# Kernel optimization log

Hardware: AMD Instinct MI355X
Metric: run time of the kernel (lower is better)

The kernel has to match this reference:

```python
import jax, jax.numpy as jnp
import numpy as np

G, V_PER, E_PER = 512, 400, 800
N, E = G * V_PER, G * E_PER
NF, H, F, OUT = 128, 64, 8, 64  # n_features, filtration_hidden, n_filtrations, out_dim


def _p(k, shape, fan_in):
    return jax.random.normal(k, shape, jnp.float32) * (1.0 / np.sqrt(fan_in))


def setup_inputs() -> dict:
    key = jax.random.key(0)
    ks = jax.random.split(key, 24)
    x = jax.random.normal(ks[0], (N, NF), jnp.float32)
    pos = jax.random.normal(ks[1], (N, 3), jnp.float32)
    # per-graph random edges, no self loops (dedup'ed single-direction edge list)
    src_l = jax.random.randint(ks[2], (E,), 0, V_PER)
    off = jax.random.randint(ks[3], (E,), 1, V_PER)
    dst_l = (src_l + off) % V_PER
    g = jnp.arange(E, dtype=jnp.int32) // E_PER
    edge_index = jnp.stack([g * V_PER + src_l, g * V_PER + dst_l]).astype(jnp.int32)
    vertex_slices = (jnp.arange(G + 1, dtype=jnp.int32) * V_PER)
    edge_slices = (jnp.arange(G + 1, dtype=jnp.int32) * E_PER)
    batch = jnp.repeat(jnp.arange(G, dtype=jnp.int32), V_PER)
    return {
        'x': x, 'pos': pos, 'edge_index': edge_index,
        'vertex_slices': vertex_slices, 'edge_slices': edge_slices, 'batch': batch,
        'W1': _p(ks[4], (NF, H), NF), 'b1': jnp.zeros((H,), jnp.float32),
        'W2': _p(ks[5], (H, F), H), 'b2': jnp.zeros((F,), jnp.float32),
        'We1': _p(ks[6], (NF + 1, H), NF + 1), 'be1': jnp.zeros((H,), jnp.float32),
        'We2': _p(ks[7], (H, F), H), 'be2': jnp.zeros((F,), jnp.float32),
        'Wd0': _p(ks[8], (F * 4, OUT), F * 4), 'bd0': jnp.zeros((OUT,), jnp.float32),
        'Wd1': _p(ks[9], (4, OUT), 4), 'bd1': jnp.zeros((OUT,), jnp.float32),
        'bn_gamma': jnp.ones((OUT,), jnp.float32), 'bn_beta': jnp.zeros((OUT,), jnp.float32),
        'Wo1': _p(ks[10], (OUT, OUT), OUT), 'bo1': jnp.zeros((OUT,), jnp.float32),
        'Wo2': _p(ks[11], (OUT, OUT), OUT), 'bo2': jnp.zeros((OUT,), jnp.float32),
    }


def reference(x, pos, edge_index, vertex_slices, edge_slices, batch,
              W1, b1, W2, b2, We1, be1, We2, be2,
              Wd0, bd0, Wd1, bd1, bn_gamma, bn_beta, Wo1, bo1, Wo2, bo2):
    n_graphs = vertex_slices.shape[0] - 1
    src, dst = edge_index[0], edge_index[1]
    mlp = lambda h, Wa, ba, Wb, bb: jax.nn.sigmoid(jnp.maximum(h @ Wa + ba, 0.0) @ Wb + bb)
    # vertex filtrations [N, F]
    fv = mlp(x, W1, b1, W2, b2)
    # edge filtrations: gather endpoint features + euclidean distance, small MLP [E, F]
    dist = jnp.sqrt(jnp.sum((pos[src] - pos[dst]) ** 2, axis=-1))
    fe = mlp(jnp.concatenate([x[src] + x[dst], dist[:, None]], axis=-1), We1, be1, We2, be2)
    # dim-0 rephine tuples (vectorizable surrogate for the CPU union-find pairing):
    # per vertex, death = min incident edge filtration, gamma = max incident edge
    # filtration; isolated vertices -> 1.0 (mirrors the NaN -> 1.0 fixup).
    dmin = jnp.full((x.shape[0], fe.shape[1]), jnp.inf, fe.dtype).at[src].min(fe).at[dst].min(fe)
    dmin = jnp.where(jnp.isinf(dmin), 1.0, dmin)
    dmax = jnp.full((x.shape[0], fe.shape[1]), -jnp.inf, fe.dtype).at[src].max(fe).at[dst].max(fe)
    dmax = jnp.where(jnp.isinf(dmax), 1.0, dmax)
    # raw (b, d, g) -> reorder [0, 2, 1] -> prepend 0  =>  (0, b, g, d), shape [N, F, 4]
    pers0 = jnp.stack([jnp.zeros_like(fv), fv, dmax, dmin], axis=-1)
    # DeepSetLayer0: Linear then scatter-mean over graphs -> [G, OUT]
    lin0 = pers0.reshape(x.shape[0], -1) @ Wd0 + bd0
    cnt_v = jax.ops.segment_sum(jnp.ones((x.shape[0],), lin0.dtype), batch, num_segments=n_graphs)
    x0 = jax.ops.segment_sum(lin0, batch, num_segments=n_graphs) / cnt_v[:, None]
    # dim-1: cycle edges = edges beyond the spanning-tree count per graph. After the
    # original's nonzero -> 1.0 assignment the dim-1 tuples are binary (0,1,1,1).
    eidx = jnp.arange(src.shape[0], dtype=jnp.int32)
    batch_e = jnp.searchsorted(edge_slices, eidx, side='right').astype(jnp.int32) - 1
    e_local = eidx - edge_slices[batch_e]
    nv = vertex_slices[batch_e + 1] - vertex_slices[batch_e]
    cyc = (e_local >= nv - 1).astype(lin0.dtype)  # [E]
    row = cyc[:, None] * jnp.array([0.0, 1.0, 1.0, 1.0], lin0.dtype)
    lin1 = row @ Wd1 + bd1  # [E, OUT]
    num = jax.ops.segment_sum(cyc[:, None] * lin1, batch_e, num_segments=n_graphs)
    den = jax.ops.segment_sum(cyc, batch_e, num_segments=n_graphs)
    x1 = jnp.where(den[:, None] > 0, num / jnp.maximum(den, 1.0)[:, None], 0.0)
    # identical across the F filtrations (binary tuples), so mean over F == x1
    h = x0 + x1
    # BatchNorm1d (training-mode batch stats, fresh affine params)
    mu = h.mean(axis=0)
    var = jnp.mean((h - mu) ** 2, axis=0)
    h = (h - mu) / jnp.sqrt(var + 1e-5) * bn_gamma + bn_beta
    # out MLP
    return jnp.maximum(h @ Wo1 + bo1, 0.0) @ Wo2 + bo2
```

## Files before the change

### kernel.cpp

```cpp
#include <hip/hip_runtime.h>
#include <math.h>

#define NV 204800
#define NE 409600
#define NG 512
#define V_PER 400
#define E_PER 800

#define BE 128
#define KT 32

__global__ __launch_bounds__(256)
void k_vertex_mlp(const float* __restrict__ x, const float* __restrict__ W1,
                  const float* __restrict__ b1, const float* __restrict__ W2,
                  const float* __restrict__ b2, float* __restrict__ fv) {
  __shared__ float Wt[KT][64];
  __shared__ float xt[KT][BE];
  __shared__ float W2s[64 * 8];

  const int tid = threadIdx.x;
  const long vb = (long)blockIdx.x * BE;

  if (tid < 128) ((float4*)W2s)[tid] = ((const float4*)W2)[tid];

  const int v = tid >> 1, h = tid & 1;
  const int jg = tid & 7, eg = tid >> 3;

  const float4 bb0 = *(const float4*)(b1 + jg * 8);
  const float4 bb1 = *(const float4*)(b1 + jg * 8 + 4);
  const float4 b2a = *(const float4*)b2;
  const float4 b2b = *(const float4*)(b2 + 4);

  float acc[4][8];
  #pragma unroll
  for (int i = 0; i < 4; ++i) {
    acc[i][0] = bb0.x; acc[i][1] = bb0.y; acc[i][2] = bb0.z; acc[i][3] = bb0.w;
    acc[i][4] = bb1.x; acc[i][5] = bb1.y; acc[i][6] = bb1.z; acc[i][7] = bb1.w;
  }

  #pragma unroll 1
  for (int t = 0; t < 4; ++t) {
    {
      const float4* src = (const float4*)(x + (vb + v) * 128 + t * KT + h * 16);
      const float4 a0 = src[0], a1 = src[1], a2 = src[2], a3 = src[3];
      const float4 wA = ((const float4*)(W1 + t * KT * 64))[tid];
      const float4 wB = ((const float4*)(W1 + t * KT * 64))[tid + 256];
      const int r = h * 16;
      xt[r + 0][v] = a0.x; xt[r + 1][v] = a0.y; xt[r + 2][v] = a0.z; xt[r + 3][v] = a0.w;
      xt[r + 4][v] = a1.x; xt[r + 5][v] = a1.y; xt[r + 6][v] = a1.z; xt[r + 7][v] = a1.w;
      xt[r + 8][v] = a2.x; xt[r + 9][v] = a2.y; xt[r +10][v] = a2.z; xt[r +11][v] = a2.w;
      xt[r +12][v] = a3.x; xt[r +13][v] = a3.y; xt[r +14][v] = a3.z; xt[r +15][v] = a3.w;
      ((float4*)&Wt[0][0])[tid] = wA;
      ((float4*)&Wt[0][0])[tid + 256] = wB;
    }
    __syncthreads();
    #pragma unroll
    for (int kk = 0; kk < KT; ++kk) {
      const float4 av = *(const float4*)&xt[kk][eg * 4];
      const float4 w0 = *(const float4*)&Wt[kk][jg * 8];
      const float4 w1 = *(const float4*)&Wt[kk][jg * 8 + 4];
      const float a[4] = {av.x, av.y, av.z, av.w};
      const float w[8] = {w0.x, w0.y, w0.z, w0.w, w1.x, w1.y, w1.z, w1.w};
      #pragma unroll
      for (int i = 0; i < 4; ++i)
        #pragma unroll
        for (int jj = 0; jj < 8; ++jj) acc[i][jj] = fmaf(a[i], w[jj], acc[i][jj]);
    }
    __syncthreads();
  }

  float p[4][8];
  #pragma unroll
  for (int i = 0; i < 4; ++i)
    #pragma unroll
    for (int o = 0; o < 8; ++o) p[i][o] = 0.f;
  #pragma unroll
  for (int jj = 0; jj < 8; ++jj) {
    const float4 w20 = *(const float4*)&W2s[(jg * 8 + jj) * 8];
    const float4 w21 = *(const float4*)&W2s[(jg * 8 + jj) * 8 + 4];
    const float w2r[8] = {w20.x, w20.y, w20.z, w20.w, w21.x, w21.y, w21.z, w21.w};
    #pragma unroll
    for (int i = 0; i < 4; ++i) {
      const float hv = fmaxf(acc[i][jj], 0.f);
      #pragma unroll
      for (int o = 0; o < 8; ++o) p[i][o] = fmaf(hv, w2r[o], p[i][o]);
    }
  }
  #pragma unroll
  for (int m = 1; m <= 4; m <<= 1)
    #pragma unroll
    for (int i = 0; i < 4; ++i)
      #pragma unroll
      for (int o = 0; o < 8; ++o) p[i][o] += __shfl_xor(p[i][o], m, 64);

  if (jg < 4) {
    const long e2 = vb + eg * 4 + jg;
    const float b2r[8] = {b2a.x, b2a.y, b2a.z, b2a.w, b2b.x, b2b.y, b2b.z, b2b.w};
    float vout[8];
    #pragma unroll
    for (int o = 0; o < 8; ++o) vout[o] = 1.0f / (1.0f + __expf(-(p[jg][o] + b2r[o])));
    *(float4*)&fv[e2 * 8]     = make_float4(vout[0], vout[1], vout[2], vout[3]);
    *(float4*)&fv[e2 * 8 + 4] = make_float4(vout[4], vout[5], vout[6], vout[7]);
  }
}

__global__ __launch_bounds__(256)
void k_edge_mlp(const float* __restrict__ x, const float* __restrict__ pos,
                const int* __restrict__ srcp, const int* __restrict__ dstp,
                const float* __restrict__ We1, const float* __restrict__ be1,
                const float* __restrict__ We2, const float* __restrict__ be2,
                float* __restrict__ fe) {
  __shared__ float Wt[KT][64];
  __shared__ float xt[KT][BE];
  __shared__ float W2s[64 * 8];
  __shared__ float ds[BE];

  const int tid = threadIdx.x;
  const int bid = blockIdx.x;
  const int lb = (bid & 7) * (NE / BE / 8) + (bid >> 3);
  const long eb = (long)lb * BE;

  if (tid < 128) ((float4*)W2s)[tid] = ((const float4*)We2)[tid];

  const int e = tid >> 1, h = tid & 1;
  const int jg = tid & 7, eg = tid >> 3;
  const int s = srcp[eb + e], d = dstp[eb + e];

  const float4 bb0 = *(const float4*)(be1 + jg * 8);
  const float4 bb1 = *(const float4*)(be1 + jg * 8 + 4);
  const float4 wd0 = *(const float4*)(We1 + 128 * 64 + jg * 8);
  const float4 wd1 = *(const float4*)(We1 + 128 * 64 + jg * 8 + 4);
  const float4 b2a = *(const float4*)be2;
  const float4 b2b = *(const float4*)(be2 + 4);

  float acc[4][8];
  #pragma unroll
  for (int i = 0; i < 4; ++i) {
    acc[i][0] = bb0.x; acc[i][1] = bb0.y; acc[i][2] = bb0.z; acc[i][3] = bb0.w;
    acc[i][4] = bb1.x; acc[i][5] = bb1.y; acc[i][6] = bb1.z; acc[i][7] = bb1.w;
  }

  if (tid < BE) {
    const int s2 = srcp[eb + tid], d2 = dstp[eb + tid];
    const float dx = pos[s2 * 3 + 0] - pos[d2 * 3 + 0];
    const float dy = pos[s2 * 3 + 1] - pos[d2 * 3 + 1];
    const float dz = pos[s2 * 3 + 2] - pos[d2 * 3 + 2];
    ds[tid] = sqrtf(dx * dx + dy * dy + dz * dz);
  }

  #pragma unroll 1
  for (int t = 0; t < 4; ++t) {
    {
      const float4* ps = (const float4*)(x + (long)s * 128 + t * KT + h * 16);
      const float4* pd = (const float4*)(x + (long)d * 128 + t * KT + h * 16);
      const float4 a0 = ps[0], a1 = ps[1], a2 = ps[2], a3 = ps[3];
      const float4 c0 = pd[0], c1 = pd[1], c2 = pd[2], c3 = pd[3];
      const float4 wA = ((const float4*)(We1 + t * KT * 64))[tid];
      const float4 wB = ((const float4*)(We1 + t * KT * 64))[tid + 256];
      const int r = h * 16;
      xt[r + 0][e] = a0.x + c0.x; xt[r + 1][e] = a0.y + c0.y;
      xt[r + 2][e] = a0.z + c0.z; xt[r + 3][e] = a0.w + c0.w;
      xt[r + 4][e] = a1.x + c1.x; xt[r + 5][e] = a1.y + c1.y;
      xt[r + 6][e] = a1.z + c1.z; xt[r + 7][e] = a1.w + c1.w;
      xt[r + 8][e] = a2.x + c2.x; xt[r + 9][e] = a2.y + c2.y;
      xt[r +10][e] = a2.z + c2.z; xt[r +11][e] = a2.w + c2.w;
      xt[r +12][e] = a3.x + c3.x; xt[r +13][e] = a3.y + c3.y;
      xt[r +14][e] = a3.z + c3.z; xt[r +15][e] = a3.w + c3.w;
      ((float4*)&Wt[0][0])[tid] = wA;
      ((float4*)&Wt[0][0])[tid + 256] = wB;
    }
    __syncthreads();
    #pragma unroll
    for (int kk = 0; kk < KT; ++kk) {
      const float4 av = *(const float4*)&xt[kk][eg * 4];
      const float4 w0 = *(const float4*)&Wt[kk][jg * 8];
      const float4 w1 = *(const float4*)&Wt[kk][jg * 8 + 4];
      const float a[4] = {av.x, av.y, av.z, av.w};
      const float w[8] = {w0.x, w0.y, w0.z, w0.w, w1.x, w1.y, w1.z, w1.w};
      #pragma unroll
      for (int i = 0; i < 4; ++i)
        #pragma unroll
        for (int jj = 0; jj < 8; ++jj) acc[i][jj] = fmaf(a[i], w[jj], acc[i][jj]);
    }
    __syncthreads();
  }

  {
    const float wdl[8] = {wd0.x, wd0.y, wd0.z, wd0.w, wd1.x, wd1.y, wd1.z, wd1.w};
    #pragma unroll
    for (int i = 0; i < 4; ++i) {
      const float dv = ds[eg * 4 + i];
      #pragma unroll
      for (int jj = 0; jj < 8; ++jj) acc[i][jj] = fmaf(dv, wdl[jj], acc[i][jj]);
    }
  }

  float p[4][8];
  #pragma unroll
  for (int i = 0; i < 4; ++i)
    #pragma unroll
    for (int o = 0; o < 8; ++o) p[i][o] = 0.f;
  #pragma unroll
  for (int jj = 0; jj < 8; ++jj) {
    const float4 w20 = *(const float4*)&W2s[(jg * 8 + jj) * 8];
    const float4 w21 = *(const float4*)&W2s[(jg * 8 + jj) * 8 + 4];
    const float w2r[8] = {w20.x, w20.y, w20.z, w20.w, w21.x, w21.y, w21.z, w21.w};
    #pragma unroll
    for (int i = 0; i < 4; ++i) {
      const float hv = fmaxf(acc[i][jj], 0.f);
      #pragma unroll
      for (int o = 0; o < 8; ++o) p[i][o] = fmaf(hv, w2r[o], p[i][o]);
    }
  }
  #pragma unroll
  for (int m = 1; m <= 4; m <<= 1)
    #pragma unroll
    for (int i = 0; i < 4; ++i)
      #pragma unroll
      for (int o = 0; o < 8; ++o) p[i][o] += __shfl_xor(p[i][o], m, 64);

  if (jg < 4) {
    const long e2 = eb + eg * 4 + jg;
    const float b2r[8] = {b2a.x, b2a.y, b2a.z, b2a.w, b2b.x, b2b.y, b2b.z, b2b.w};
    float vout[8];
    #pragma unroll
    for (int o = 0; o < 8; ++o) vout[o] = 1.0f / (1.0f + __expf(-(p[jg][o] + b2r[o])));
    *(float4*)&fe[e2 * 8]     = make_float4(vout[0], vout[1], vout[2], vout[3]);
    *(float4*)&fe[e2 * 8 + 4] = make_float4(vout[4], vout[5], vout[6], vout[7]);
  }
}

__global__ __launch_bounds__(256, 2)
void k_graph_reduce(const float* __restrict__ fv, const float* __restrict__ fe,
                    const int* __restrict__ srcp, const int* __restrict__ dstp,
                    const float* __restrict__ Wd0, const float* __restrict__ bd0,
                    const float* __restrict__ Wd1, const float* __restrict__ bd1,
                    float* __restrict__ hbuf) {
  __shared__ unsigned dminS[8 * V_PER];
  __shared__ unsigned dmaxS[8 * V_PER];
  __shared__ float red[256];
  __shared__ float sums[3][8];
  const int tid = threadIdx.x;
  const int g = blockIdx.x;

  for (int i = tid; i < 8 * V_PER; i += 256) {
    dminS[i] = 0x7F800000u;
    dmaxS[i] = 0u;
  }
  __syncthreads();

  const int eb = g * E_PER;
  const int vb = g * V_PER;
  for (int e = tid; e < E_PER; e += 256) {
    const int ls = srcp[eb + e] - vb;
    const int ld = dstp[eb + e] - vb;
    const uint4 f0 = ((const uint4*)(fe + (long)(eb + e) * 8))[0];
    const uint4 f1 = ((const uint4*)(fe + (long)(eb + e) * 8))[1];
    const unsigned fb[8] = {f0.x, f0.y, f0.z, f0.w, f1.x, f1.y, f1.z, f1.w};
    #pragma unroll
    for (int f = 0; f < 8; ++f) {
      atomicMin(&dminS[f * V_PER + ls], fb[f]);
      atomicMax(&dmaxS[f * V_PER + ls], fb[f]);
      atomicMin(&dminS[f * V_PER + ld], fb[f]);
      atomicMax(&dmaxS[f * V_PER + ld], fb[f]);
    }
  }
  __syncthreads();

  const int f = tid & 7;
  float sfv = 0.f, smin = 0.f, smax = 0.f;
  for (int v = tid >> 3; v < V_PER; v += 32) {
    sfv += fv[(long)(vb + v) * 8 + f];
    const unsigned mn = dminS[f * V_PER + v];
    if (mn == 0x7F800000u) { smin += 1.0f; smax += 1.0f; }
    else { smin += __uint_as_float(mn); smax += __uint_as_float(dmaxS[f * V_PER + v]); }
  }
  red[tid] = sfv; __syncthreads();
  for (int s = 128; s >= 8; s >>= 1) { if (tid < s) red[tid] += red[tid + s]; __syncthreads(); }
  if (tid < 8) sums[0][tid] = red[tid];
  __syncthreads();
  red[tid] = smax; __syncthreads();
  for (int s = 128; s >= 8; s >>= 1) { if (tid < s) red[tid] += red[tid + s]; __syncthreads(); }
  if (tid < 8) sums[1][tid] = red[tid];
  __syncthreads();
  red[tid] = smin; __syncthreads();
  for (int s = 128; s >= 8; s >>= 1) { if (tid < s) red[tid] += red[tid + s]; __syncthreads(); }
  if (tid < 8) sums[2][tid] = red[tid];
  __syncthreads();

  if (tid < 64) {
    const int o = tid;
    const float inv = 1.0f / (float)V_PER;
    float acc = bd0[o];
    #pragma unroll
    for (int ff = 0; ff < 8; ++ff) {
      acc = fmaf(sums[0][ff] * inv, Wd0[(4 * ff + 1) * 64 + o], acc);
      acc = fmaf(sums[1][ff] * inv, Wd0[(4 * ff + 2) * 64 + o], acc);
      acc = fmaf(sums[2][ff] * inv, Wd0[(4 * ff + 3) * 64 + o], acc);
    }
    const float x1 = Wd1[64 + o] + Wd1[128 + o] + Wd1[192 + o] + bd1[o];
    hbuf[g * 64 + o] = acc + x1;
  }
}

__global__ __launch_bounds__(256)
void k_bn_stats(const float* __restrict__ hbuf, float* __restrict__ mu,
                float* __restrict__ rstd) {
  __shared__ float rs[256], rs2[256];
  const int tid = threadIdx.x;
  const int c = tid & 63, rg = tid >> 6;
  float s = 0.f, s2 = 0.f;
  for (int r = rg * 128; r < rg * 128 + 128; ++r) {
    const float v = hbuf[r * 64 + c];
    s += v; s2 += v * v;
  }
  rs[tid] = s; rs2[tid] = s2; __syncthreads();
  if (tid < 128) { rs[tid] += rs[tid + 128]; rs2[tid] += rs2[tid + 128]; }
  __syncthreads();
  if (tid < 64) {
    const float st = rs[tid] + rs[tid + 64];
    const float st2 = rs2[tid] + rs2[tid + 64];
    const float m = st / 512.0f;
    const float var = st2 / 512.0f - m * m;
    mu[tid] = m;
    rstd[tid] = rsqrtf(var + 1e-5f);
  }
}

__global__ __launch_bounds__(256)
void k_out_mlp(const float* __restrict__ hbuf, const float* __restrict__ mu,
               const float* __restrict__ rstd, const float* __restrict__ gam,
               const float* __restrict__ bet, const float* __restrict__ Wo1,
               const float* __restrict__ bo1, const float* __restrict__ Wo2,
               const float* __restrict__ bo2, float* __restrict__ out) {
  __shared__ float W1s[64 * 64], W2s[64 * 64];
  __shared__ float hn[4][64], t1[4][64];
  __shared__ float mus[64], rstds[64], gs[64], bs[64], b1s[64], b2s[64];
  const int tid = threadIdx.x;
  for (int i = tid; i < 4096; i += 256) { W1s[i] = Wo1[i]; W2s[i] = Wo2[i]; }
  if (tid < 64) {
    mus[tid] = mu[tid]; rstds[tid] = rstd[tid]; gs[tid] = gam[tid];
    bs[tid] = bet[tid]; b1s[tid] = bo1[tid]; b2s[tid] = bo2[tid];
  }
  __syncthreads();
  const int r = tid >> 6, o = tid & 63;
  for (int it = 0; it < 4; ++it) {
    const int row = blockIdx.x * 16 + it * 4 + r;
    hn[r][o] = (hbuf[row * 64 + o] - mus[o]) * rstds[o] * gs[o] + bs[o];
    __syncthreads();
    float a = b1s[o];
    #pragma unroll 8
    for (int i = 0; i < 64; ++i) a = fmaf(hn[r][i], W1s[i * 64 + o], a);
    t1[r][o] = fmaxf(a, 0.f);
    __syncthreads();
    float a2 = b2s[o];
    #pragma unroll 8
    for (int i = 0; i < 64; ++i) a2 = fmaf(t1[r][i], W2s[i * 64 + o], a2);
    out[row * 64 + o] = a2;
    __syncthreads();
  }
}

extern "C" void kernel_launch(void* const* d_in, const int* in_sizes, int n_in,
                              void* d_out, int out_size, void* d_ws, size_t ws_size,
                              hipStream_t stream) {
  const float* x   = (const float*)d_in[0];
  const float* pos = (const float*)d_in[1];
  const int*   ei  = (const int*)d_in[2];
  const float* W1  = (const float*)d_in[6];
  const float* b1  = (const float*)d_in[7];
  const float* W2  = (const float*)d_in[8];
  const float* b2  = (const float*)d_in[9];
  const float* We1 = (const float*)d_in[10];
  const float* be1 = (const float*)d_in[11];
  const float* We2 = (const float*)d_in[12];
  const float* be2 = (const float*)d_in[13];
  const float* Wd0 = (const float*)d_in[14];
  const float* bd0 = (const float*)d_in[15];
  const float* Wd1 = (const float*)d_in[16];
  const float* bd1 = (const float*)d_in[17];
  const float* gam = (const float*)d_in[18];
  const float* bet = (const float*)d_in[19];
  const float* Wo1 = (const float*)d_in[20];
  const float* bo1 = (const float*)d_in[21];
  const float* Wo2 = (const float*)d_in[22];
  const float* bo2 = (const float*)d_in[23];

  const int* srcp = ei;
  const int* dstp = ei + NE;

  float* fv   = (float*)d_ws;
  float* fe   = fv + (size_t)NV * 8;
  float* hb   = fe + (size_t)NE * 8;
  float* mu   = hb + NG * 64;
  float* rstd = mu + 64;

  hipLaunchKernelGGL(k_vertex_mlp, dim3(NV / BE), dim3(256), 0, stream,
                     x, W1, b1, W2, b2, fv);
  hipLaunchKernelGGL(k_edge_mlp, dim3(NE / BE), dim3(256), 0, stream,
                     x, pos, srcp, dstp, We1, be1, We2, be2, fe);
  hipLaunchKernelGGL(k_graph_reduce, dim3(NG), dim3(256), 0, stream,
                     fv, fe, srcp, dstp, Wd0, bd0, Wd1, bd1, hb);
  hipLaunchKernelGGL(k_bn_stats, dim3(1), dim3(256), 0, stream, hb, mu, rstd);
  hipLaunchKernelGGL(k_out_mlp, dim3(NG / 16), dim3(256), 0, stream,
                     hb, mu, rstd, gam, bet, Wo1, bo1, Wo2, bo2, (float*)d_out);
}
```

Before: 403.2 us.

## Project node features once with edge weights, then gather projections per edge

```diff
diff --git a/kernel.cpp b/kernel.cpp
--- a/kernel.cpp
+++ b/kernel.cpp
@@ -7,68 +7,102 @@
 #define V_PER 400
 #define E_PER 800
 
-#define BE 128
+#define BM 128
 #define KT 32
 
+__device__ __forceinline__ int wswz(int j) { return j ^ (((j >> 5) & 1) << 2); }
+
 __global__ __launch_bounds__(256)
-void k_vertex_mlp(const float* __restrict__ x, const float* __restrict__ W1,
-                  const float* __restrict__ b1, const float* __restrict__ W2,
-                  const float* __restrict__ b2, float* __restrict__ fv) {
-  __shared__ float Wt[KT][64];
-  __shared__ float xt[KT][BE];
+void k_proj(const float* __restrict__ x, const float* __restrict__ W1,
+            const float* __restrict__ b1, const float* __restrict__ W2,
+            const float* __restrict__ b2, const float* __restrict__ We1,
+            float* __restrict__ fv, float* __restrict__ y2) {
+  __shared__ __align__(16) char smem[33280];
+  float (*xt)[BM] = (float (*)[BM])smem;
+  float (*Wt)[BM] = (float (*)[BM])(smem + KT * BM * 4);
+  float (*hs)[65] = (float (*)[65])smem;
   __shared__ float W2s[64 * 8];
 
   const int tid = threadIdx.x;
-  const long vb = (long)blockIdx.x * BE;
+  const long vb = (long)blockIdx.x * BM;
 
   if (tid < 128) ((float4*)W2s)[tid] = ((const float4*)W2)[tid];
 
   const int v = tid >> 1, h = tid & 1;
-  const int jg = tid & 7, eg = tid >> 3;
-
-  const float4 bb0 = *(const float4*)(b1 + jg * 8);
-  const float4 bb1 = *(const float4*)(b1 + jg * 8 + 4);
-  const float4 b2a = *(const float4*)b2;
-  const float4 b2b = *(const float4*)(b2 + 4);
-
-  float acc[4][8];
-  #pragma unroll
-  for (int i = 0; i < 4; ++i) {
-    acc[i][0] = bb0.x; acc[i][1] = bb0.y; acc[i][2] = bb0.z; acc[i][3] = bb0.w;
-    acc[i][4] = bb1.x; acc[i][5] = bb1.y; acc[i][6] = bb1.z; acc[i][7] = bb1.w;
-  }
+  const int jg = tid & 15, rg = tid >> 4;
+
+  const int wb0 = wswz(jg * 8);
+  const int wb1 = wswz(jg * 8 + 4);
+
+  float acc[8][8];
+  #pragma unroll
+  for (int i = 0; i < 8; ++i)
+    #pragma unroll
+    for (int j = 0; j < 8; ++j) acc[i][j] = 0.f;
 
   #pragma unroll 1
   for (int t = 0; t < 4; ++t) {
     {
       const float4* src = (const float4*)(x + (vb + v) * 128 + t * KT + h * 16);
       const float4 a0 = src[0], a1 = src[1], a2 = src[2], a3 = src[3];
-      const float4 wA = ((const float4*)(W1 + t * KT * 64))[tid];
-      const float4 wB = ((const float4*)(W1 + t * KT * 64))[tid + 256];
       const int r = h * 16;
       xt[r + 0][v] = a0.x; xt[r + 1][v] = a0.y; xt[r + 2][v] = a0.z; xt[r + 3][v] = a0.w;
       xt[r + 4][v] = a1.x; xt[r + 5][v] = a1.y; xt[r + 6][v] = a1.z; xt[r + 7][v] = a1.w;
       xt[r + 8][v] = a2.x; xt[r + 9][v] = a2.y; xt[r +10][v] = a2.z; xt[r +11][v] = a2.w;
       xt[r +12][v] = a3.x; xt[r +13][v] = a3.y; xt[r +14][v] = a3.z; xt[r +15][v] = a3.w;
-      ((float4*)&Wt[0][0])[tid] = wA;
-      ((float4*)&Wt[0][0])[tid + 256] = wB;
+      #pragma unroll
+      for (int q = 0; q < 2; ++q) {
+        const int idx = tid + q * 256;
+        const int kk = idx >> 4, j4 = idx & 15;
+        const float4 wa = ((const float4*)(W1 + t * KT * 64))[idx];
+        const float4 wb = ((const float4*)(We1 + t * KT * 64))[idx];
+        *(float4*)&Wt[kk][wswz(j4 * 4)] = wa;
+        *(float4*)&Wt[kk][wswz(64 + j4 * 4)] = wb;
+      }
     }
     __syncthreads();
     #pragma unroll
     for (int kk = 0; kk < KT; ++kk) {
-      const float4 av = *(const float4*)&xt[kk][eg * 4];
-      const float4 w0 = *(const float4*)&Wt[kk][jg * 8];
-      const float4 w1 = *(const float4*)&Wt[kk][jg * 8 + 4];
-      const float a[4] = {av.x, av.y, av.z, av.w};
+      const float4 av0 = *(const float4*)&xt[kk][rg * 8];
+      const float4 av1 = *(const float4*)&xt[kk][rg * 8 + 4];
+      const float4 w0 = *(const float4*)&Wt[kk][wb0];
+      const float4 w1 = *(const float4*)&Wt[kk][wb1];
+      const float a[8] = {av0.x, av0.y, av0.z, av0.w, av1.x, av1.y, av1.z, av1.w};
       const float w[8] = {w0.x, w0.y, w0.z, w0.w, w1.x, w1.y, w1.z, w1.w};
       #pragma unroll
-      for (int i = 0; i < 4; ++i)
+      for (int i = 0; i < 8; ++i)
         #pragma unroll
-        for (int jj = 0; jj < 8; ++jj) acc[i][jj] = fmaf(a[i], w[jj], acc[i][jj]);
-    }
-    __syncthreads();
-  }
-
+        for (int j = 0; j < 8; ++j) acc[i][j] = fmaf(a[i], w[j], acc[i][j]);
+    }
+    __syncthreads();
+  }
+
+  if (jg < 8) {
+    const float4 b1a = *(const float4*)(b1 + jg * 8);
+    const float4 b1b = *(const float4*)(b1 + jg * 8 + 4);
+    #pragma unroll
+    for (int i = 0; i < 8; ++i) {
+      const int row = rg * 8 + i;
+      *(float4*)&hs[row][jg * 8] = make_float4(
+          fmaxf(acc[i][0] + b1a.x, 0.f), fmaxf(acc[i][1] + b1a.y, 0.f),
+          fmaxf(acc[i][2] + b1a.z, 0.f), fmaxf(acc[i][3] + b1a.w, 0.f));
+      *(float4*)&hs[row][jg * 8 + 4] = make_float4(
+          fmaxf(acc[i][4] + b1b.x, 0.f), fmaxf(acc[i][5] + b1b.y, 0.f),
+          fmaxf(acc[i][6] + b1b.z, 0.f), fmaxf(acc[i][7] + b1b.w, 0.f));
+    }
+  } else {
+    #pragma unroll
+    for (int i = 0; i < 8; ++i) {
+      const long row = vb + rg * 8 + i;
+      *(float4*)&y2[row * 64 + (jg - 8) * 8] =
+          make_float4(acc[i][0], acc[i][1], acc[i][2], acc[i][3]);
+      *(float4*)&y2[row * 64 + (jg - 8) * 8 + 4] =
+          make_float4(acc[i][4], acc[i][5], acc[i][6], acc[i][7]);
+    }
+  }
+  __syncthreads();
+
+  const int jg2 = tid & 7, eg2 = tid >> 3;
   float p[4][8];
   #pragma unroll
   for (int i = 0; i < 4; ++i)
@@ -76,12 +110,12 @@
     for (int o = 0; o < 8; ++o) p[i][o] = 0.f;
   #pragma unroll
   for (int jj = 0; jj < 8; ++jj) {
-    const float4 w20 = *(const float4*)&W2s[(jg * 8 + jj) * 8];
-    const float4 w21 = *(const float4*)&W2s[(jg * 8 + jj) * 8 + 4];
+    const float4 w20 = *(const float4*)&W2s[(jg2 * 8 + jj) * 8];
+    const float4 w21 = *(const float4*)&W2s[(jg2 * 8 + jj) * 8 + 4];
     const float w2r[8] = {w20.x, w20.y, w20.z, w20.w, w21.x, w21.y, w21.z, w21.w};
     #pragma unroll
     for (int i = 0; i < 4; ++i) {
-      const float hv = fmaxf(acc[i][jj], 0.f);
+      const float hv = hs[eg2 * 4 + i][jg2 * 8 + jj];
       #pragma unroll
       for (int o = 0; o < 8; ++o) p[i][o] = fmaf(hv, w2r[o], p[i][o]);
     }
@@ -93,140 +127,77 @@
       #pragma unroll
       for (int o = 0; o < 8; ++o) p[i][o] += __shfl_xor(p[i][o], m, 64);
 
-  if (jg < 4) {
-    const long e2 = vb + eg * 4 + jg;
+  if (jg2 < 4) {
+    const float4 b2a = *(const float4*)b2;
+    const float4 b2b = *(const float4*)(b2 + 4);
     const float b2r[8] = {b2a.x, b2a.y, b2a.z, b2a.w, b2b.x, b2b.y, b2b.z, b2b.w};
+    const long row = vb + eg2 * 4 + jg2;
     float vout[8];
     #pragma unroll
-    for (int o = 0; o < 8; ++o) vout[o] = 1.0f / (1.0f + __expf(-(p[jg][o] + b2r[o])));
-    *(float4*)&fv[e2 * 8]     = make_float4(vout[0], vout[1], vout[2], vout[3]);
-    *(float4*)&fv[e2 * 8 + 4] = make_float4(vout[4], vout[5], vout[6], vout[7]);
+    for (int o = 0; o < 8; ++o) vout[o] = 1.0f / (1.0f + __expf(-(p[jg2][o] + b2r[o])));
+    *(float4*)&fv[row * 8]     = make_float4(vout[0], vout[1], vout[2], vout[3]);
+    *(float4*)&fv[row * 8 + 4] = make_float4(vout[4], vout[5], vout[6], vout[7]);
   }
 }
 
 __global__ __launch_bounds__(256)
-void k_edge_mlp(const float* __restrict__ x, const float* __restrict__ pos,
-                const int* __restrict__ srcp, const int* __restrict__ dstp,
-                const float* __restrict__ We1, const float* __restrict__ be1,
-                const float* __restrict__ We2, const float* __restrict__ be2,
-                float* __restrict__ fe) {
-  __shared__ float Wt[KT][64];
-  __shared__ float xt[KT][BE];
-  __shared__ float W2s[64 * 8];
-  __shared__ float ds[BE];
-
-  const int tid = threadIdx.x;
-  const int bid = blockIdx.x;
-  const int lb = (bid & 7) * (NE / BE / 8) + (bid >> 3);
-  const long eb = (long)lb * BE;
-
-  if (tid < 128) ((float4*)W2s)[tid] = ((const float4*)We2)[tid];
-
-  const int e = tid >> 1, h = tid & 1;
-  const int jg = tid & 7, eg = tid >> 3;
-  const int s = srcp[eb + e], d = dstp[eb + e];
-
-  const float4 bb0 = *(const float4*)(be1 + jg * 8);
-  const float4 bb1 = *(const float4*)(be1 + jg * 8 + 4);
-  const float4 wd0 = *(const float4*)(We1 + 128 * 64 + jg * 8);
-  const float4 wd1 = *(const float4*)(We1 + 128 * 64 + jg * 8 + 4);
+void k_edge_finish(const float* __restrict__ y2, const float* __restrict__ pos,
+                   const int* __restrict__ srcp, const int* __restrict__ dstp,
+                   const float* __restrict__ We1, const float* __restrict__ be1,
+                   const float* __restrict__ We2, const float* __restrict__ be2,
+                   float* __restrict__ fe) {
+  const int tid = threadIdx.x;
+  const int jg = tid & 7;
+  const long ebase = (long)blockIdx.x * 256;
+
+  float w2[64];
+  #pragma unroll
+  for (int q = 0; q < 16; ++q)
+    *(float4*)&w2[q * 4] = ((const float4*)(We2 + jg * 64))[q];
+  const float4 wda = *(const float4*)(We1 + 128 * 64 + jg * 8);
+  const float4 wdb = *(const float4*)(We1 + 128 * 64 + jg * 8 + 4);
+  const float4 bea = *(const float4*)(be1 + jg * 8);
+  const float4 beb = *(const float4*)(be1 + jg * 8 + 4);
+  const float wd[8] = {wda.x, wda.y, wda.z, wda.w, wdb.x, wdb.y, wdb.z, wdb.w};
+  const float be[8] = {bea.x, bea.y, bea.z, bea.w, beb.x, beb.y, beb.z, beb.w};
   const float4 b2a = *(const float4*)be2;
   const float4 b2b = *(const float4*)(be2 + 4);
 
-  float acc[4][8];
-  #pragma unroll
-  for (int i = 0; i < 4; ++i) {
-    acc[i][0] = bb0.x; acc[i][1] = bb0.y; acc[i][2] = bb0.z; acc[i][3] = bb0.w;
-    acc[i][4] = bb1.x; acc[i][5] = bb1.y; acc[i][6] = bb1.z; acc[i][7] = bb1.w;
-  }
-
-  if (tid < BE) {
-    const int s2 = srcp[eb + tid], d2 = dstp[eb + tid];
-    const float dx = pos[s2 * 3 + 0] - pos[d2 * 3 + 0];
-    const float dy = pos[s2 * 3 + 1] - pos[d2 * 3 + 1];
-    const float dz = pos[s2 * 3 + 2] - pos[d2 * 3 + 2];
-    ds[tid] = sqrtf(dx * dx + dy * dy + dz * dz);
-  }
-
   #pragma unroll 1
-  for (int t = 0; t < 4; ++t) {
-    {
-      const float4* ps = (const float4*)(x + (long)s * 128 + t * KT + h * 16);
-      const float4* pd = (const float4*)(x + (long)d * 128 + t * KT + h * 16);
-      const float4 a0 = ps[0], a1 = ps[1], a2 = ps[2], a3 = ps[3];
-      const float4 c0 = pd[0], c1 = pd[1], c2 = pd[2], c3 = pd[3];
-      const float4 wA = ((const float4*)(We1 + t * KT * 64))[tid];
-      const float4 wB = ((const float4*)(We1 + t * KT * 64))[tid + 256];
-      const int r = h * 16;
-      xt[r + 0][e] = a0.x + c0.x; xt[r + 1][e] = a0.y + c0.y;
-      xt[r + 2][e] = a0.z + c0.z; xt[r + 3][e] = a0.w + c0.w;
-      xt[r + 4][e] = a1.x + c1.x; xt[r + 5][e] = a1.y + c1.y;
-      xt[r + 6][e] = a1.z + c1.z; xt[r + 7][e] = a1.w + c1.w;
-      xt[r + 8][e] = a2.x + c2.x; xt[r + 9][e] = a2.y + c2.y;
-      xt[r +10][e] = a2.z + c2.z; xt[r +11][e] = a2.w + c2.w;
-      xt[r +12][e] = a3.x + c3.x; xt[r +13][e] = a3.y + c3.y;
-      xt[r +14][e] = a3.z + c3.z; xt[r +15][e] = a3.w + c3.w;
-      ((float4*)&Wt[0][0])[tid] = wA;
-      ((float4*)&Wt[0][0])[tid + 256] = wB;
-    }
-    __syncthreads();
-    #pragma unroll
-    for (int kk = 0; kk < KT; ++kk) {
-      const float4 av = *(const float4*)&xt[kk][eg * 4];
-      const float4 w0 = *(const float4*)&Wt[kk][jg * 8];
-      const float4 w1 = *(const float4*)&Wt[kk][jg * 8 + 4];
-      const float a[4] = {av.x, av.y, av.z, av.w};
-      const float w[8] = {w0.x, w0.y, w0.z, w0.w, w1.x, w1.y, w1.z, w1.w};
-      #pragma unroll
-      for (int i = 0; i < 4; ++i)
-        #pragma unroll
-        for (int jj = 0; jj < 8; ++jj) acc[i][jj] = fmaf(a[i], w[jj], acc[i][jj]);
-    }
-    __syncthreads();
-  }
-
-  {
-    const float wdl[8] = {wd0.x, wd0.y, wd0.z, wd0.w, wd1.x, wd1.y, wd1.z, wd1.w};
-    #pragma unroll
-    for (int i = 0; i < 4; ++i) {
-      const float dv = ds[eg * 4 + i];
-      #pragma unroll
-      for (int jj = 0; jj < 8; ++jj) acc[i][jj] = fmaf(dv, wdl[jj], acc[i][jj]);
-    }
-  }
-
-  float p[4][8];
-  #pragma unroll
-  for (int i = 0; i < 4; ++i)
-    #pragma unroll
-    for (int o = 0; o < 8; ++o) p[i][o] = 0.f;
-  #pragma unroll
-  for (int jj = 0; jj < 8; ++jj) {
-    const float4 w20 = *(const float4*)&W2s[(jg * 8 + jj) * 8];
-    const float4 w21 = *(const float4*)&W2s[(jg * 8 + jj) * 8 + 4];
-    const float w2r[8] = {w20.x, w20.y, w20.z, w20.w, w21.x, w21.y, w21.z, w21.w};
-    #pragma unroll
-    for (int i = 0; i < 4; ++i) {
-      const float hv = fmaxf(acc[i][jj], 0.f);
-      #pragma unroll
-      for (int o = 0; o < 8; ++o) p[i][o] = fmaf(hv, w2r[o], p[i][o]);
-    }
-  }
-  #pragma unroll
-  for (int m = 1; m <= 4; m <<= 1)
-    #pragma unroll
-    for (int i = 0; i < 4; ++i)
-      #pragma unroll
-      for (int o = 0; o < 8; ++o) p[i][o] += __shfl_xor(p[i][o], m, 64);
-
-  if (jg < 4) {
-    const long e2 = eb + eg * 4 + jg;
-    const float b2r[8] = {b2a.x, b2a.y, b2a.z, b2a.w, b2b.x, b2b.y, b2b.z, b2b.w};
-    float vout[8];
-    #pragma unroll
-    for (int o = 0; o < 8; ++o) vout[o] = 1.0f / (1.0f + __expf(-(p[jg][o] + b2r[o])));
-    *(float4*)&fe[e2 * 8]     = make_float4(vout[0], vout[1], vout[2], vout[3]);
-    *(float4*)&fe[e2 * 8 + 4] = make_float4(vout[4], vout[5], vout[6], vout[7]);
+  for (int ps = 0; ps < 8; ++ps) {
+    const long e = ebase + ps * 32 + (tid >> 3);
+    const int s = srcp[e], d = dstp[e];
+    const float4 a0 = *(const float4*)(y2 + (long)s * 64 + jg * 8);
+    const float4 a1 = *(const float4*)(y2 + (long)s * 64 + jg * 8 + 4);
+    const float4 c0 = *(const float4*)(y2 + (long)d * 64 + jg * 8);
+    const float4 c1 = *(const float4*)(y2 + (long)d * 64 + jg * 8 + 4);
+    const float dx = pos[s * 3 + 0] - pos[d * 3 + 0];
+    const float dy = pos[s * 3 + 1] - pos[d * 3 + 1];
+    const float dz = pos[s * 3 + 2] - pos[d * 3 + 2];
+    const float dist = sqrtf(dx * dx + dy * dy + dz * dz);
+    float hh[8] = {a0.x + c0.x, a0.y + c0.y, a0.z + c0.z, a0.w + c0.w,
+                   a1.x + c1.x, a1.y + c1.y, a1.z + c1.z, a1.w + c1.w};
+    float p[8];
+    #pragma unroll
+    for (int o = 0; o < 8; ++o) p[o] = 0.f;
+    #pragma unroll
+    for (int jj = 0; jj < 8; ++jj) {
+      const float hv = fmaxf(fmaf(dist, wd[jj], hh[jj] + be[jj]), 0.f);
+      #pragma unroll
+      for (int o = 0; o < 8; ++o) p[o] = fmaf(hv, w2[jj * 8 + o], p[o]);
+    }
+    #pragma unroll
+    for (int m = 1; m <= 4; m <<= 1)
+      #pragma unroll
+      for (int o = 0; o < 8; ++o) p[o] += __shfl_xor(p[o], m, 64);
+    if (jg == 0) {
+      float vout[8];
+      const float b2r[8] = {b2a.x, b2a.y, b2a.z, b2a.w, b2b.x, b2b.y, b2b.z, b2b.w};
+      #pragma unroll
+      for (int o = 0; o < 8; ++o) vout[o] = 1.0f / (1.0f + __expf(-(p[o] + b2r[o])));
+      *(float4*)&fe[e * 8]     = make_float4(vout[0], vout[1], vout[2], vout[3]);
+      *(float4*)&fe[e * 8 + 4] = make_float4(vout[4], vout[5], vout[6], vout[7]);
+    }
   }
 }
 
@@ -394,11 +365,12 @@
   float* hb   = fe + (size_t)NE * 8;
   float* mu   = hb + NG * 64;
   float* rstd = mu + 64;
-
-  hipLaunchKernelGGL(k_vertex_mlp, dim3(NV / BE), dim3(256), 0, stream,
-                     x, W1, b1, W2, b2, fv);
-  hipLaunchKernelGGL(k_edge_mlp, dim3(NE / BE), dim3(256), 0, stream,
-                     x, pos, srcp, dstp, We1, be1, We2, be2, fe);
+  float* y2   = rstd + 64;
+
+  hipLaunchKernelGGL(k_proj, dim3(NV / BM), dim3(256), 0, stream,
+                     x, W1, b1, W2, b2, We1, fv, y2);
+  hipLaunchKernelGGL(k_edge_finish, dim3(NE / 256), dim3(256), 0, stream,
+                     y2, pos, srcp, dstp, We1, be1, We2, be2, fe);
   hipLaunchKernelGGL(k_graph_reduce, dim3(NG), dim3(256), 0, stream,
                      fv, fe, srcp, dstp, Wd0, bd0, Wd1, bd1, hb);
   hipLaunchKernelGGL(k_bn_stats, dim3(1), dim3(256), 0, stream, hb, mu, rstd);
```

Result: faster. 370.3 us (-8.2%).
